# Performance work log

Hardware: AMD Instinct MI355X
Metric: run time of the kernel (lower is better)

Reference implementation:

```python
import jax, jax.numpy as jnp
import numpy as np

H, NH, HD = 1024, 16, 64
B, T, S = 2, 1024, 3
NOISE, STEP, TEMP, NSTEPS = 0.1, 0.01, 1.0, 5
LN_EPS = 1e-5


def setup_inputs() -> dict:
    key = jax.random.key(0)
    ks = jax.random.split(key, 9)
    return {
        "queries": jax.random.normal(ks[0], (B, NH, T, HD), jnp.float32),
        "keys": jax.random.normal(ks[1], (B, NH, T, HD), jnp.float32),
        "values": jax.random.normal(ks[2], (B, NH, T, HD), jnp.float32),
        "hidden_states": jax.random.normal(ks[3], (B, T, H), jnp.float32),
        "W1": jax.random.normal(ks[4], (H, H), jnp.float32) * 0.02,
        "b1": jnp.zeros((H,), jnp.float32),
        "ln_g": jnp.ones((H,), jnp.float32),
        "ln_b": jnp.zeros((H,), jnp.float32),
        "W2": jax.random.normal(ks[5], (H, H), jnp.float32) * 0.02,
        "b2": jnp.zeros((H,), jnp.float32),
        "hyp_noise": jax.random.normal(ks[6], (S, B, NH, T, HD), jnp.float32),
        "ref_noise": jax.random.normal(ks[7], (S, NSTEPS - 1, B, NH, T, HD), jnp.float32),
    }


def _attention_energy(q, k, v):
    # q: [S,B,H,T,D]; k,v: [B,H,T,D] -> energy [S,B]
    scores = jnp.einsum('sbhtd,bhud->sbhtu', q, k) / jnp.sqrt(jnp.float32(q.shape[-1]))
    attn = jax.nn.softmax(scores, axis=-1)
    out = jnp.einsum('sbhtu,bhud->sbhtd', attn, v)
    out_mag = jnp.linalg.norm(out, axis=-1).mean(axis=(2, 3))          # [S,B]
    entropy = -(attn * jnp.log(attn + 1e-8)).sum(axis=-1).mean(axis=(2, 3))
    align = (q * k[None]).sum(axis=-1).mean(axis=(2, 3))
    return out_mag - 0.1 * entropy - 0.05 * align


def reference(queries, keys, values, hidden_states, W1, b1, ln_g, ln_b, W2, b2,
              hyp_noise, ref_noise):
    # query_predictor: Linear -> LayerNorm -> ReLU -> Linear
    x = hidden_states @ W1.T + b1
    mu = x.mean(axis=-1, keepdims=True)
    var = ((x - mu) ** 2).mean(axis=-1, keepdims=True)
    x = (x - mu) / jnp.sqrt(var + LN_EPS) * ln_g + ln_b
    x = jax.nn.relu(x)
    ctx = x @ W2.T + b2                                   # [B,T,H]
    ctx = ctx.reshape(B, T, NH, HD).transpose(0, 2, 1, 3) # [B,NH,T,HD]

    # exploration hypotheses, refined jointly over the sample axis
    q = queries[None] + hyp_noise * NOISE                 # [S,B,NH,T,HD]
    for step in range(NSTEPS):
        q = q - STEP * (q - ctx[None])                    # PCN prediction-error update
        if step < NSTEPS - 1:
            q = q + ref_noise[:, step] * 0.01

    energies = _attention_energy(q, keys, values)         # [S,B]
    probs = jax.nn.softmax(-energies / TEMP, axis=0)      # [S,B]
    selected = jnp.einsum('sb,sbhtd->bhtd', probs, q)     # softmax-weighted mix
    return selected, keys, values
```

## Files before the change

kernel.cpp:

```cpp
#include <hip/hip_runtime.h>
#include <hip/hip_bf16.h>
#include <math.h>

#define NB 2
#define NHH 16
#define TT 1024
#define HDD 64
#define NSS 3
#define HH 1024
#define MMR 2048

typedef float f4 __attribute__((ext_vector_type(4)));
typedef short bf16x8 __attribute__((ext_vector_type(8)));
typedef unsigned short u16;
typedef u16 u16x4 __attribute__((ext_vector_type(4)));

__device__ inline u16 f2bf(float f) {
    union { float f; unsigned u; } v; v.f = f;
    unsigned r = (v.u + 0x7FFFu + ((v.u >> 16) & 1u)) >> 16;
    return (u16)r;
}
__device__ inline float bf2f(u16 u) {
    union { unsigned u; float f; } v; v.u = ((unsigned)u) << 16;
    return v.f;
}

__device__ inline float red16sum(float v) {
    v += __shfl_xor(v, 1);
    v += __shfl_xor(v, 2);
    v += __shfl_xor(v, 4);
    v += __shfl_xor(v, 8);
    return v;
}
__device__ inline float red64sum(float v) {
    v += __shfl_xor(v, 1);
    v += __shfl_xor(v, 2);
    v += __shfl_xor(v, 4);
    v += __shfl_xor(v, 8);
    v += __shfl_xor(v, 16);
    v += __shfl_xor(v, 32);
    return v;
}

__global__ __launch_bounds__(256) void k_cvt4(const float* __restrict__ s0, u16* __restrict__ d0,
                                              const float* __restrict__ s1, u16* __restrict__ d1,
                                              const float* __restrict__ s2, u16* __restrict__ d2,
                                              const float* __restrict__ s3, u16* __restrict__ d3,
                                              float* __restrict__ outk) {
    int b = blockIdx.x;
    if (b >= 4096) {
        int i = (b - 4096) * 256 + threadIdx.x;
        f4 v = ((const f4*)s3)[i];
        ((f4*)outk)[i] = v;
        u16x4 o;
        o[0] = f2bf(v[0] * 0.125f); o[1] = f2bf(v[1] * 0.125f);
        o[2] = f2bf(v[2] * 0.125f); o[3] = f2bf(v[3] * 0.125f);
        ((u16x4*)d3)[i] = o;
        return;
    }
    const float* s; u16* d; int base;
    if (b < 2048)      { s = s0; d = d0; base = 0; }
    else if (b < 3072) { s = s1; d = d1; base = 2048; }
    else               { s = s2; d = d2; base = 3072; }
    int i = (b - base) * 256 + threadIdx.x;
    f4 v = ((const f4*)s)[i];
    u16x4 o;
    o[0] = f2bf(v[0]); o[1] = f2bf(v[1]); o[2] = f2bf(v[2]); o[3] = f2bf(v[3]);
    ((u16x4*)d)[i] = o;
}

__global__ __launch_bounds__(256) void k_vtrans(const float* __restrict__ V,
                                                u16* __restrict__ Vt,
                                                float* __restrict__ outv) {
    __shared__ float tile[64][65];
    int bh = blockIdx.y, t0 = blockIdx.x * 64;
    int r = threadIdx.x >> 2, c0 = (threadIdx.x & 3) * 16;
    const float* vp = V + ((size_t)bh * TT + t0) * HDD;
#pragma unroll
    for (int j = 0; j < 16; j += 4) {
        f4 v = *(const f4*)(vp + r * HDD + c0 + j);
        tile[r][c0 + j + 0] = v[0]; tile[r][c0 + j + 1] = v[1];
        tile[r][c0 + j + 2] = v[2]; tile[r][c0 + j + 3] = v[3];
        *(f4*)(outv + ((size_t)bh * TT + t0 + r) * HDD + c0 + j) = v;
    }
    __syncthreads();
    int d = threadIdx.x >> 2, x0 = (threadIdx.x & 3) * 16;
    u16* op = Vt + ((size_t)bh * HDD + d) * TT + t0 + x0;
#pragma unroll
    for (int j = 0; j < 16; j += 4) {
        u16x4 o;
        o[0] = f2bf(tile[x0 + j + 0][d]); o[1] = f2bf(tile[x0 + j + 1][d]);
        o[2] = f2bf(tile[x0 + j + 2][d]); o[3] = f2bf(tile[x0 + j + 3][d]);
        *(u16x4*)(op + j) = o;
    }
}

template <int EPI>
__global__ __launch_bounds__(256) void k_gemm_bt(const u16* __restrict__ A,
                                                 const u16* __restrict__ Bm,
                                                 const float* __restrict__ bias,
                                                 float* __restrict__ out) {
    const int K = 1024, N = 1024;
    int w = threadIdx.x >> 6, l = threadIdx.x & 63, lr = l & 15, lg = l >> 4;
    int m0 = blockIdx.y * 64 + w * 16;
    int n0 = blockIdx.x * 64;
    const u16* ap = A + (size_t)(m0 + lr) * K + lg * 8;
    const u16* bp = Bm + (size_t)(n0 + lr) * K + lg * 8;
    f4 z4 = {0.f, 0.f, 0.f, 0.f};
    f4 acc[4] = {z4, z4, z4, z4};
#pragma unroll 2
    for (int kk = 0; kk < K; kk += 32) {
        bf16x8 a  = *(const bf16x8*)(ap + kk);
        bf16x8 b0 = *(const bf16x8*)(bp + kk);
        bf16x8 b1 = *(const bf16x8*)(bp + 16 * K + kk);
        bf16x8 b2 = *(const bf16x8*)(bp + 32 * K + kk);
        bf16x8 b3 = *(const bf16x8*)(bp + 48 * K + kk);
        acc[0] = __builtin_amdgcn_mfma_f32_16x16x32_bf16(a, b0, acc[0], 0, 0, 0);
        acc[1] = __builtin_amdgcn_mfma_f32_16x16x32_bf16(a, b1, acc[1], 0, 0, 0);
        acc[2] = __builtin_amdgcn_mfma_f32_16x16x32_bf16(a, b2, acc[2], 0, 0, 0);
        acc[3] = __builtin_amdgcn_mfma_f32_16x16x32_bf16(a, b3, acc[3], 0, 0, 0);
    }
#pragma unroll
    for (int cf = 0; cf < 4; ++cf) {
        int col = n0 + cf * 16 + lr;
        float bs = bias[col];
#pragma unroll
        for (int r = 0; r < 4; ++r) {
            int row = m0 + lg * 4 + r;
            float v = acc[cf][r] + bs;
            if (EPI == 0) {
                out[(size_t)row * N + col] = v;
            } else {
                int b = row >> 10, t = row & 1023, nh = col >> 6, hd = col & 63;
                out[(((size_t)(b * NHH + nh)) * TT + t) * HDD + hd] = v;
            }
        }
    }
}

__global__ __launch_bounds__(256) void k_lnrelu(const float* __restrict__ X,
                                                const float* __restrict__ g,
                                                const float* __restrict__ bta,
                                                u16* __restrict__ xr) {
    int row = blockIdx.x;
    f4 v = ((const f4*)(X + (size_t)row * HH))[threadIdx.x];
    float s = v[0] + v[1] + v[2] + v[3];
    float s2 = v[0] * v[0] + v[1] * v[1] + v[2] * v[2] + v[3] * v[3];
    s = red64sum(s);
    s2 = red64sum(s2);
    __shared__ float red[8];
    int w = threadIdx.x >> 6, l = threadIdx.x & 63;
    if (l == 0) { red[w] = s; red[w + 4] = s2; }
    __syncthreads();
    float S1 = red[0] + red[1] + red[2] + red[3];
    float S2 = red[4] + red[5] + red[6] + red[7];
    float mu = S1 * (1.0f / 1024.0f);
    float var = S2 * (1.0f / 1024.0f) - mu * mu;
    float rstd = rsqrtf(var + 1e-5f);
    f4 gv = ((const f4*)g)[threadIdx.x];
    f4 bv = ((const f4*)bta)[threadIdx.x];
    u16x4 o;
#pragma unroll
    for (int j = 0; j < 4; ++j) {
        float y = (v[j] - mu) * rstd * gv[j] + bv[j];
        y = fmaxf(y, 0.f);
        o[j] = f2bf(y);
    }
    ((u16x4*)(xr + (size_t)row * HH))[threadIdx.x] = o;
}

__global__ __launch_bounds__(256) void k_qform(const float* __restrict__ que,
                                               const float* __restrict__ hyp,
                                               const float* __restrict__ rn,
                                               const float* __restrict__ ctx,
                                               u16* __restrict__ qq) {
    const int NQ4 = 524288;
    int bx = blockIdx.x;
    int s = bx >> 10;
    int i = ((bx & 1023) * 256 + threadIdx.x) * 2;
    const float A5 = 0.9509900499f, CC = 1.0f - A5, CH = 0.1f * A5;
    const float C0 = 0.0096059601f, C1 = 0.0097029900f, C2 = 0.0098010000f, C3 = 0.0099f;
    const f4* qp  = (const f4*)que;
    const f4* cp  = (const f4*)ctx;
    const f4* hp  = (const f4*)hyp + (size_t)s * NQ4;
    const f4* r0p = (const f4*)rn + (size_t)(s * 4 + 0) * NQ4;
    const f4* r1p = (const f4*)rn + (size_t)(s * 4 + 1) * NQ4;
    const f4* r2p = (const f4*)rn + (size_t)(s * 4 + 2) * NQ4;
    const f4* r3p = (const f4*)rn + (size_t)(s * 4 + 3) * NQ4;
    u16 ob[8];
#pragma unroll
    for (int j = 0; j < 2; ++j) {
        f4 qv = qp[i + j];
        f4 cv = cp[i + j];
        f4 h  = __builtin_nontemporal_load(hp + i + j);
        f4 r0 = __builtin_nontemporal_load(r0p + i + j);
        f4 r1 = __builtin_nontemporal_load(r1p + i + j);
        f4 r2 = __builtin_nontemporal_load(r2p + i + j);
        f4 r3 = __builtin_nontemporal_load(r3p + i + j);
        f4 v = A5 * qv + CC * cv + CH * h + C0 * r0 + C1 * r1 + C2 * r2 + C3 * r3;
        ob[j * 4 + 0] = f2bf(v[0]); ob[j * 4 + 1] = f2bf(v[1]);
        ob[j * 4 + 2] = f2bf(v[2]); ob[j * 4 + 3] = f2bf(v[3]);
    }
    *(int4*)(qq + (size_t)s * 4 * NQ4 + (size_t)i * 4) = *(const int4*)ob;
}

__global__ __launch_bounds__(256, 3) void k_attn(const u16* __restrict__ qq,
                                                 const u16* __restrict__ Kb,
                                                 const u16* __restrict__ Vt,
                                                 float* __restrict__ part) {
    int bi = blockIdx.x;
    int qt2 = bi & 7, h = (bi >> 3) & 15, sb = bi >> 7;
    int b = sb & 1;
    int bh = b * NHH + h;
    int w = threadIdx.x >> 6, l = threadIdx.x & 63, lr = l & 15, lg = l >> 4;
    int t0 = qt2 * 128;
    f4 z4 = {0.f, 0.f, 0.f, 0.f};

    __shared__ u16 Ks[4096];
    __shared__ u16 Vs[4096];
    __shared__ u16 plds[8][1024];

    bf16x8 aq[2][2];
#pragma unroll
    for (int qr = 0; qr < 2; ++qr) {
        const u16* qrow = qq + (((size_t)(sb * NHH + h)) * TT + t0 + w * 32 + qr * 16 + lr) * HDD;
        aq[qr][0] = *(const bf16x8*)(qrow + lg * 8);
        aq[qr][1] = *(const bf16x8*)(qrow + 32 + lg * 8);
    }

    const u16* kbase = Kb + (size_t)bh * TT * HDD;
    const u16* vbase = Vt + (size_t)bh * HDD * TT;
    int u0 = threadIdx.x, u1 = threadIdx.x + 256;
    const u16* kg0 = kbase + u0 * 8;
    const u16* kg1 = kbase + u1 * 8;
    const u16* vg0 = vbase + (size_t)(u0 >> 3) * TT + (u0 & 7) * 8;
    const u16* vg1 = vbase + (size_t)(u1 >> 3) * TT + (u1 & 7) * 8;
    int ko0 = (u0 >> 3) * 128 + (((u0 & 7) ^ ((u0 >> 3) & 7)) << 4);
    int ko1 = (u1 >> 3) * 128 + (((u1 & 7) ^ ((u1 >> 3) & 7)) << 4);
    char* KsB = (char*)Ks;
    char* VsB = (char*)Vs;

    int4 kr0 = *(const int4*)(kg0);
    int4 kr1 = *(const int4*)(kg1);
    int4 vr0 = *(const int4*)(vg0);
    int4 vr1 = *(const int4*)(vg1);

    f4 acco[2][4] = {{z4, z4, z4, z4}, {z4, z4, z4, z4}};
    float zrow[2][4] = {{0.f, 0.f, 0.f, 0.f}, {0.f, 0.f, 0.f, 0.f}};
    float wrow[2][4] = {{0.f, 0.f, 0.f, 0.f}, {0.f, 0.f, 0.f, 0.f}};

    for (int kt = 0; kt < 16; ++kt) {
        __syncthreads();
        *(int4*)(KsB + ko0) = kr0;
        *(int4*)(KsB + ko1) = kr1;
        *(int4*)(VsB + ko0) = vr0;
        *(int4*)(VsB + ko1) = vr1;
        if (kt < 15) {
            kr0 = *(const int4*)(kg0 + (kt + 1) * 4096);
            kr1 = *(const int4*)(kg1 + (kt + 1) * 4096);
            vr0 = *(const int4*)(vg0 + (kt + 1) * 64);
            vr1 = *(const int4*)(vg1 + (kt + 1) * 64);
        }
        __syncthreads();

        f4 sc[2][4];
#pragma unroll
        for (int cf = 0; cf < 4; ++cf) {
            int row = cf * 16 + lr, rs = row & 7;
            bf16x8 bk0 = *(const bf16x8*)(KsB + row * 128 + ((lg ^ rs) << 4));
            bf16x8 bk1 = *(const bf16x8*)(KsB + row * 128 + (((4 + lg) ^ rs) << 4));
            f4 t0a = __builtin_amdgcn_mfma_f32_16x16x32_bf16(aq[0][0], bk0, z4, 0, 0, 0);
            sc[0][cf] = __builtin_amdgcn_mfma_f32_16x16x32_bf16(aq[0][1], bk1, t0a, 0, 0, 0);
            f4 t1a = __builtin_amdgcn_mfma_f32_16x16x32_bf16(aq[1][0], bk0, z4, 0, 0, 0);
            sc[1][cf] = __builtin_amdgcn_mfma_f32_16x16x32_bf16(aq[1][1], bk1, t1a, 0, 0, 0);
        }

#pragma unroll
        for (int qr = 0; qr < 2; ++qr) {
            u16* pl = &plds[w * 2 + qr][0];
#pragma unroll
            for (int cf = 0; cf < 4; ++cf) {
#pragma unroll
                for (int r = 0; r < 4; ++r) {
                    float sv = sc[qr][cf][r];
                    float pe = __expf(sv);
                    zrow[qr][r] += pe;
                    wrow[qr][r] = fmaf(pe, sv, wrow[qr][r]);
                    int prow = lg * 4 + r;
                    pl[(prow * 64 + cf * 16 + lr) ^ ((prow & 7) << 3)] = f2bf(pe);
                }
            }
        }
        bf16x8 pa[2][2];
#pragma unroll
        for (int qr = 0; qr < 2; ++qr) {
            const u16* pl = &plds[w * 2 + qr][0];
            pa[qr][0] = *(const bf16x8*)&pl[(lr * 64 + lg * 8) ^ ((lr & 7) << 3)];
            pa[qr][1] = *(const bf16x8*)&pl[(lr * 64 + 32 + lg * 8) ^ ((lr & 7) << 3)];
        }
#pragma unroll
        for (int cf = 0; cf < 4; ++cf) {
            int row = cf * 16 + lr, rs = row & 7;
            bf16x8 bv0 = *(const bf16x8*)(VsB + row * 128 + ((lg ^ rs) << 4));
            bf16x8 bv1 = *(const bf16x8*)(VsB + row * 128 + (((4 + lg) ^ rs) << 4));
            acco[0][cf] = __builtin_amdgcn_mfma_f32_16x16x32_bf16(pa[0][0], bv0, acco[0][cf], 0, 0, 0);
            acco[0][cf] = __builtin_amdgcn_mfma_f32_16x16x32_bf16(pa[0][1], bv1, acco[0][cf], 0, 0, 0);
            acco[1][cf] = __builtin_amdgcn_mfma_f32_16x16x32_bf16(pa[1][0], bv0, acco[1][cf], 0, 0, 0);
            acco[1][cf] = __builtin_amdgcn_mfma_f32_16x16x32_bf16(pa[1][1], bv1, acco[1][cf], 0, 0, 0);
        }
    }

    float magw = 0.f, entw = 0.f;
#pragma unroll
    for (int qr = 0; qr < 2; ++qr) {
#pragma unroll
        for (int r = 0; r < 4; ++r) {
            float zz = red16sum(zrow[qr][r]);
            float ww = red16sum(wrow[qr][r]);
            float ssq = acco[qr][0][r] * acco[qr][0][r] + acco[qr][1][r] * acco[qr][1][r] +
                        acco[qr][2][r] * acco[qr][2][r] + acco[qr][3][r] * acco[qr][3][r];
            ssq = red16sum(ssq);
            float inv = 1.0f / zz;
            magw += sqrtf(ssq) * inv;
            entw += __logf(zz) - ww * inv;
        }
    }
    magw += __shfl_xor(magw, 16); magw += __shfl_xor(magw, 32);
    entw += __shfl_xor(entw, 16); entw += __shfl_xor(entw, 32);

    int arow = threadIdx.x >> 1, ah = (threadIdx.x & 1) * 32;
    const u16* qa = qq + (((size_t)(sb * NHH + h)) * TT + t0 + arow) * HDD + ah;
    const u16* ka = Kb + (((size_t)bh) * TT + t0 + arow) * HDD + ah;
    float al = 0.f;
#pragma unroll
    for (int j = 0; j < 32; j += 4) {
        u16x4 qv4 = *(const u16x4*)(qa + j);
        u16x4 kv4 = *(const u16x4*)(ka + j);
        al += bf2f(qv4[0]) * bf2f(kv4[0]) + bf2f(qv4[1]) * bf2f(kv4[1]) +
              bf2f(qv4[2]) * bf2f(kv4[2]) + bf2f(qv4[3]) * bf2f(kv4[3]);
    }
    al = red64sum(al) * 8.0f;

    __shared__ float red[4][3];
    if (l == 0) { red[w][0] = magw; red[w][1] = entw; red[w][2] = al; }
    __syncthreads();
    if (threadIdx.x == 0) {
        part[bi * 3 + 0] = red[0][0] + red[1][0] + red[2][0] + red[3][0];
        part[bi * 3 + 1] = red[0][1] + red[1][1] + red[2][1] + red[3][1];
        part[bi * 3 + 2] = red[0][2] + red[1][2] + red[2][2] + red[3][2];
    }
}

__global__ void k_finalize(const float* __restrict__ part, float* __restrict__ probs) {
    int w = threadIdx.x >> 6, l = threadIdx.x & 63;
    __shared__ float eng[6];
    if (w < 6) {
        float a0 = 0.f, a1 = 0.f, a2 = 0.f;
        for (int i = l; i < 128; i += 64) {
            const float* pp = part + (size_t)(w * 128 + i) * 3;
            a0 += pp[0]; a1 += pp[1]; a2 += pp[2];
        }
        a0 = red64sum(a0); a1 = red64sum(a1); a2 = red64sum(a2);
        if (l == 0) {
            const float inv = 1.0f / 16384.0f;
            eng[w] = a0 * inv - 0.1f * (a1 * inv) - 0.05f * (a2 * inv);
        }
    }
    __syncthreads();
    if (threadIdx.x < 2) {
        int b = threadIdx.x;
        float e0 = -eng[0 + b], e1 = -eng[2 + b], e2 = -eng[4 + b];
        float mx = fmaxf(e0, fmaxf(e1, e2));
        float x0 = __expf(e0 - mx), x1 = __expf(e1 - mx), x2 = __expf(e2 - mx);
        float inv = 1.0f / (x0 + x1 + x2);
        probs[0 + b] = x0 * inv;
        probs[2 + b] = x1 * inv;
        probs[4 + b] = x2 * inv;
    }
}

__global__ __launch_bounds__(256) void k_select(const u16* __restrict__ qq,
                                                const float* __restrict__ probs,
                                                float* __restrict__ out) {
    const int NQ4 = 524288;
    int i = blockIdx.x * 256 + threadIdx.x;
    int b = i >> 18;
    float p0 = probs[0 + b], p1 = probs[2 + b], p2 = probs[4 + b];
    u16x4 a0 = ((const u16x4*)qq)[i];
    u16x4 a1 = ((const u16x4*)qq)[NQ4 + i];
    u16x4 a2 = ((const u16x4*)qq)[2 * NQ4 + i];
    f4 v;
#pragma unroll
    for (int j = 0; j < 4; ++j)
        v[j] = p0 * bf2f(a0[j]) + p1 * bf2f(a1[j]) + p2 * bf2f(a2[j]);
    ((f4*)out)[i] = v;
}

extern "C" void kernel_launch(void* const* d_in, const int* in_sizes, int n_in,
                              void* d_out, int out_size, void* d_ws, size_t ws_size,
                              hipStream_t stream) {
    const float* queries = (const float*)d_in[0];
    const float* keys    = (const float*)d_in[1];
    const float* values  = (const float*)d_in[2];
    const float* hs      = (const float*)d_in[3];
    const float* W1      = (const float*)d_in[4];
    const float* b1      = (const float*)d_in[5];
    const float* ln_g    = (const float*)d_in[6];
    const float* ln_b    = (const float*)d_in[7];
    const float* W2      = (const float*)d_in[8];
    const float* b2      = (const float*)d_in[9];
    const float* hyp     = (const float*)d_in[10];
    const float* rn      = (const float*)d_in[11];
    float* out = (float*)d_out;
    char* ws = (char*)d_ws;

    const size_t MB = 1024ull * 1024ull;
    u16*   qq16 = (u16*)(ws);
    u16*   hs_b = (u16*)(ws + 0 * MB);
    u16*   w1_b = (u16*)(ws + 4 * MB);
    u16*   w2_b = (u16*)(ws + 6 * MB);
    float* X    = (float*)(ws + 8 * MB);
    u16*   xr   = (u16*)(ws + 16 * MB);
    float* ctx  = (float*)(ws + 24 * MB);
    u16*   k_b  = (u16*)(ws + 32 * MB);
    u16*   vt_b = (u16*)(ws + 36 * MB);
    float* part = (float*)(ws + 40 * MB);
    float* probs= (float*)(ws + 40 * MB + 65536);

    k_cvt4<<<6144, 256, 0, stream>>>(hs, hs_b, W1, w1_b, W2, w2_b, keys, k_b,
                                     out + 2097152);
    k_vtrans<<<dim3(16, 32), 256, 0, stream>>>(values, vt_b, out + 4194304);

    k_gemm_bt<0><<<dim3(16, 32), 256, 0, stream>>>(hs_b, w1_b, b1, X);
    k_lnrelu<<<2048, 256, 0, stream>>>(X, ln_g, ln_b, xr);
    k_gemm_bt<1><<<dim3(16, 32), 256, 0, stream>>>(xr, w2_b, b2, ctx);

    k_qform<<<3072, 256, 0, stream>>>(queries, hyp, rn, ctx, qq16);
    k_attn<<<768, 256, 0, stream>>>(qq16, k_b, vt_b, part);
    k_finalize<<<1, 384, 0, stream>>>(part, probs);
    k_select<<<2048, 256, 0, stream>>>(qq16, probs, out);
}
```

Before: 179.2 us.

## Fuse query formation into the attention kernel and drop the separate qform pass

```diff
diff --git a/kernel.cpp b/kernel.cpp
--- a/kernel.cpp
+++ b/kernel.cpp
@@ -169,48 +169,17 @@
     ((u16x4*)(xr + (size_t)row * HH))[threadIdx.x] = o;
 }
 
-__global__ __launch_bounds__(256) void k_qform(const float* __restrict__ que,
-                                               const float* __restrict__ hyp,
-                                               const float* __restrict__ rn,
-                                               const float* __restrict__ ctx,
-                                               u16* __restrict__ qq) {
-    const int NQ4 = 524288;
-    int bx = blockIdx.x;
-    int s = bx >> 10;
-    int i = ((bx & 1023) * 256 + threadIdx.x) * 2;
-    const float A5 = 0.9509900499f, CC = 1.0f - A5, CH = 0.1f * A5;
-    const float C0 = 0.0096059601f, C1 = 0.0097029900f, C2 = 0.0098010000f, C3 = 0.0099f;
-    const f4* qp  = (const f4*)que;
-    const f4* cp  = (const f4*)ctx;
-    const f4* hp  = (const f4*)hyp + (size_t)s * NQ4;
-    const f4* r0p = (const f4*)rn + (size_t)(s * 4 + 0) * NQ4;
-    const f4* r1p = (const f4*)rn + (size_t)(s * 4 + 1) * NQ4;
-    const f4* r2p = (const f4*)rn + (size_t)(s * 4 + 2) * NQ4;
-    const f4* r3p = (const f4*)rn + (size_t)(s * 4 + 3) * NQ4;
-    u16 ob[8];
-#pragma unroll
-    for (int j = 0; j < 2; ++j) {
-        f4 qv = qp[i + j];
-        f4 cv = cp[i + j];
-        f4 h  = __builtin_nontemporal_load(hp + i + j);
-        f4 r0 = __builtin_nontemporal_load(r0p + i + j);
-        f4 r1 = __builtin_nontemporal_load(r1p + i + j);
-        f4 r2 = __builtin_nontemporal_load(r2p + i + j);
-        f4 r3 = __builtin_nontemporal_load(r3p + i + j);
-        f4 v = A5 * qv + CC * cv + CH * h + C0 * r0 + C1 * r1 + C2 * r2 + C3 * r3;
-        ob[j * 4 + 0] = f2bf(v[0]); ob[j * 4 + 1] = f2bf(v[1]);
-        ob[j * 4 + 2] = f2bf(v[2]); ob[j * 4 + 3] = f2bf(v[3]);
-    }
-    *(int4*)(qq + (size_t)s * 4 * NQ4 + (size_t)i * 4) = *(const int4*)ob;
-}
-
-__global__ __launch_bounds__(256, 3) void k_attn(const u16* __restrict__ qq,
+__global__ __launch_bounds__(256, 3) void k_attn(const float* __restrict__ que,
+                                                 const float* __restrict__ ctx,
+                                                 const float* __restrict__ hyp,
+                                                 const float* __restrict__ rn,
                                                  const u16* __restrict__ Kb,
                                                  const u16* __restrict__ Vt,
+                                                 u16* __restrict__ qq,
                                                  float* __restrict__ part) {
     int bi = blockIdx.x;
     int qt2 = bi & 7, h = (bi >> 3) & 15, sb = bi >> 7;
-    int b = sb & 1;
+    int s = sb >> 1, b = sb & 1;
     int bh = b * NHH + h;
     int w = threadIdx.x >> 6, l = threadIdx.x & 63, lr = l & 15, lg = l >> 4;
     int t0 = qt2 * 128;
@@ -220,12 +189,43 @@
     __shared__ u16 Vs[4096];
     __shared__ u16 plds[8][1024];
 
+    const float A5 = 0.9509900499f, CC = 1.0f - A5, CH = 0.1f * A5;
+    const float C0 = 0.0096059601f, C1 = 0.0097029900f, C2 = 0.0098010000f, C3 = 0.0099f;
+    const float* quep = que + ((size_t)bh * TT) * HDD;
+    const float* ctxp = ctx + ((size_t)bh * TT) * HDD;
+    const float* hypp = hyp + ((size_t)(sb * NHH + h) * TT) * HDD;
+    const float* rn0p = rn + ((size_t)(((s * 4 + 0) * 2 + b) * NHH + h) * TT) * HDD;
+    const float* rn1p = rn + ((size_t)(((s * 4 + 1) * 2 + b) * NHH + h) * TT) * HDD;
+    const float* rn2p = rn + ((size_t)(((s * 4 + 2) * 2 + b) * NHH + h) * TT) * HDD;
+    const float* rn3p = rn + ((size_t)(((s * 4 + 3) * 2 + b) * NHH + h) * TT) * HDD;
+    u16* qqp = qq + ((size_t)(sb * NHH + h) * TT) * HDD;
+
     bf16x8 aq[2][2];
 #pragma unroll
     for (int qr = 0; qr < 2; ++qr) {
-        const u16* qrow = qq + (((size_t)(sb * NHH + h)) * TT + t0 + w * 32 + qr * 16 + lr) * HDD;
-        aq[qr][0] = *(const bf16x8*)(qrow + lg * 8);
-        aq[qr][1] = *(const bf16x8*)(qrow + 32 + lg * 8);
+        size_t ro = (size_t)(t0 + w * 32 + qr * 16 + lr) * HDD;
+#pragma unroll
+        for (int c = 0; c < 2; ++c) {
+            int d0 = c * 32 + lg * 8;
+            f4 va, vb;
+#pragma unroll
+            for (int half = 0; half < 2; ++half) {
+                size_t off = ro + d0 + half * 4;
+                f4 v = A5 * *(const f4*)(quep + off);
+                v += CC * *(const f4*)(ctxp + off);
+                v += CH * __builtin_nontemporal_load((const f4*)(hypp + off));
+                v += C0 * __builtin_nontemporal_load((const f4*)(rn0p + off));
+                v += C1 * __builtin_nontemporal_load((const f4*)(rn1p + off));
+                v += C2 * __builtin_nontemporal_load((const f4*)(rn2p + off));
+                v += C3 * __builtin_nontemporal_load((const f4*)(rn3p + off));
+                if (half == 0) va = v; else vb = v;
+            }
+            union { bf16x8 f; u16 u[8]; int4 i4; } o;
+#pragma unroll
+            for (int j = 0; j < 4; ++j) { o.u[j] = f2bf(va[j]); o.u[4 + j] = f2bf(vb[j]); }
+            aq[qr][c] = o.f;
+            *(int4*)(qqp + ro + d0) = o.i4;
+        }
     }
 
     const u16* kbase = Kb + (size_t)bh * TT * HDD;
@@ -329,7 +329,7 @@
     entw += __shfl_xor(entw, 16); entw += __shfl_xor(entw, 32);
 
     int arow = threadIdx.x >> 1, ah = (threadIdx.x & 1) * 32;
-    const u16* qa = qq + (((size_t)(sb * NHH + h)) * TT + t0 + arow) * HDD + ah;
+    const u16* qa = qqp + (size_t)(t0 + arow) * HDD + ah;
     const u16* ka = Kb + (((size_t)bh) * TT + t0 + arow) * HDD + ah;
     float al = 0.f;
 #pragma unroll
@@ -435,8 +435,7 @@
     k_lnrelu<<<2048, 256, 0, stream>>>(X, ln_g, ln_b, xr);
     k_gemm_bt<1><<<dim3(16, 32), 256, 0, stream>>>(xr, w2_b, b2, ctx);
 
-    k_qform<<<3072, 256, 0, stream>>>(queries, hyp, rn, ctx, qq16);
-    k_attn<<<768, 256, 0, stream>>>(qq16, k_b, vt_b, part);
+    k_attn<<<768, 256, 0, stream>>>(queries, ctx, hyp, rn, k_b, vt_b, qq16, part);
     k_finalize<<<1, 384, 0, stream>>>(part, probs);
     k_select<<<2048, 256, 0, stream>>>(qq16, probs, out);
 }
```

After: 175.7 us. 1.02x faster.
